# Kernel tuning notes

Hardware: AMD Instinct MI355X
Metric: run time of the kernel (lower is better)

Reference implementation:

```python
import jax, jax.numpy as jnp
import numpy as np


def grid_sample_bilinear(feat, grid):
    """Bilinear grid_sample, align_corners=False, zeros padding.
    feat: [B, C, H, W]; grid: [B, N, 2] with (x, y) in [-1, 1]. Returns [B, C, N].
    """
    B, C, H, W = feat.shape
    gx, gy = grid[..., 0], grid[..., 1]
    # unnormalize (align_corners=False): pixel = ((g + 1) * size - 1) / 2
    ix = ((gx + 1.0) * W - 1.0) * 0.5
    iy = ((gy + 1.0) * H - 1.0) * 0.5
    x0 = jnp.floor(ix)
    y0 = jnp.floor(iy)
    x1 = x0 + 1.0
    y1 = y0 + 1.0
    wx1 = ix - x0
    wx0 = 1.0 - wx1
    wy1 = iy - y0
    wy0 = 1.0 - wy1
    featf = feat.reshape(B, C, H * W)

    def corner(xi, yi, w):
        valid = (xi >= 0) & (xi <= W - 1) & (yi >= 0) & (yi <= H - 1)
        xi_c = jnp.clip(xi, 0, W - 1).astype(jnp.int32)
        yi_c = jnp.clip(yi, 0, H - 1).astype(jnp.int32)
        idx = yi_c * W + xi_c                                  # [B, N]
        vals = jnp.take_along_axis(featf, idx[:, None, :], axis=2)  # [B, C, N]
        return vals * (w * valid.astype(feat.dtype))[:, None, :]

    return (corner(x0, y0, wx0 * wy0) + corner(x1, y0, wx1 * wy0)
            + corner(x0, y1, wx0 * wy1) + corner(x1, y1, wx1 * wy1))


def setup_inputs() -> dict:
    key = jax.random.key(0)
    ks = jax.random.split(key, 8)
    B_T, C, H, W = 128, 256, 64, 64
    J = 17
    n_heads, n_points = 8, 4
    HP = n_heads * n_points
    video_features = jax.random.normal(ks[0], (B_T, C, H, W), dtype=jnp.float32)
    reference_points = jax.random.uniform(ks[1], (B_T, J, 2), dtype=jnp.float32,
                                          minval=-1.0, maxval=1.0)
    # offset predictor: Linear(C -> HP*2); weights init small like the module
    W_off = 0.01 * jax.random.normal(ks[2], (C, HP * 2), dtype=jnp.float32)
    b_off = 0.01 * jax.random.normal(ks[3], (HP * 2,), dtype=jnp.float32)
    # weight predictor: Linear(C -> HP)
    W_w = 0.01 * jax.random.normal(ks[4], (C, HP), dtype=jnp.float32)
    b_w = jnp.zeros((HP,), dtype=jnp.float32)
    # output projection: Linear(C -> C), xavier-ish scale
    W_out = jax.random.normal(ks[5], (C, C), dtype=jnp.float32) * (1.0 / np.sqrt(C))
    b_out = jnp.zeros((C,), dtype=jnp.float32)
    return {"video_features": video_features, "reference_points": reference_points,
            "W_off": W_off, "b_off": b_off, "W_w": W_w, "b_w": b_w,
            "W_out": W_out, "b_out": b_out}


def reference(video_features, reference_points, W_off, b_off, W_w, b_w, W_out, b_out):
    B, C, H, W = video_features.shape
    J = reference_points.shape[1]
    HP = W_w.shape[1]  # n_heads * n_points
    # initial queries: sample features at reference points -> [B, J, C]
    q = grid_sample_bilinear(video_features, reference_points).transpose(0, 2, 1)
    # learned fractional offsets: [B, J, HP, 2]
    offsets = (q @ W_off + b_off).reshape(B, J, HP, 2)
    # softmax attention weights over all heads*points: [B, J, HP]
    weights = jax.nn.softmax(q @ W_w + b_w, axis=-1)
    # final sampling grid, clamped to valid range: [B, J*HP, 2]
    grid = jnp.clip(reference_points[:, :, None, :] + offsets, -1.0, 1.0)
    grid = grid.reshape(B, J * HP, 2)
    # sample and weighted-sum: [B, C, J, HP] x [B, J, HP] -> [B, J, C]
    sampled = grid_sample_bilinear(video_features, grid).reshape(B, C, J, HP)
    out = jnp.einsum('bcjp,bjp->bjc', sampled, weights)
    return out @ W_out + b_out
```

## Files before the change

### kernel.cpp

```cpp
#include <hip/hip_runtime.h>

#define B_  128
#define C_  256
#define H_  64
#define W_  64
#define J_  17
#define HP_ 32
#define HW_ (H_ * W_)
#define CG_ 4

__global__ __launch_bounds__(256)
void pass12_kernel(const float* __restrict__ feat,
                   const float* __restrict__ refpts,
                   const float* __restrict__ Woff,
                   const float* __restrict__ boff,
                   const float* __restrict__ Ww,
                   const float* __restrict__ bw,
                   int4*  __restrict__ meta_idx,
                   float4* __restrict__ meta_w)
{
    __shared__ float q_lds[C_];
    __shared__ float part_off[4][64];
    __shared__ float part_w[8][32];
    __shared__ float off_lds[2 * HP_];
    __shared__ float logit_lds[HP_];

    const int bj = blockIdx.x;
    const int b  = bj / J_;
    const int j  = bj % J_;
    const int c  = threadIdx.x;

    const float rx = refpts[(b * J_ + j) * 2 + 0];
    const float ry = refpts[(b * J_ + j) * 2 + 1];

    {
        const float* featbc = feat + (size_t)(b * C_ + c) * HW_;
        float ix = (rx + 1.0f) * (0.5f * W_) - 0.5f;
        float iy = (ry + 1.0f) * (0.5f * H_) - 0.5f;
        float x0f = floorf(ix), y0f = floorf(iy);
        int x0 = (int)x0f, y0 = (int)y0f;
        int x1 = x0 + 1,  y1 = y0 + 1;
        float wx1 = ix - x0f, wx0 = 1.0f - wx1;
        float wy1 = iy - y0f, wy0 = 1.0f - wy1;
        bool vx0 = (x0 >= 0) && (x0 < W_);
        bool vx1 = (x1 >= 0) && (x1 < W_);
        bool vy0 = (y0 >= 0) && (y0 < H_);
        bool vy1 = (y1 >= 0) && (y1 < H_);
        int x0c = min(max(x0, 0), W_ - 1), x1c = min(max(x1, 0), W_ - 1);
        int y0c = min(max(y0, 0), H_ - 1), y1c = min(max(y1, 0), H_ - 1);
        float v00 = (vx0 && vy0) ? featbc[y0c * W_ + x0c] : 0.0f;
        float v10 = (vx1 && vy0) ? featbc[y0c * W_ + x1c] : 0.0f;
        float v01 = (vx0 && vy1) ? featbc[y1c * W_ + x0c] : 0.0f;
        float v11 = (vx1 && vy1) ? featbc[y1c * W_ + x1c] : 0.0f;
        q_lds[c] = v00 * (wx0 * wy0) + v10 * (wx1 * wy0)
                 + v01 * (wx0 * wy1) + v11 * (wx1 * wy1);
    }
    __syncthreads();

    {
        const int wv = c >> 6, ln = c & 63;
        float aoff = 0.0f;
        #pragma unroll 8
        for (int i = 0; i < 64; ++i) {
            const int k = wv * 64 + i;
            aoff += q_lds[k] * Woff[k * 64 + ln];
        }
        part_off[wv][ln] = aoff;
        const int h = ln >> 5, p = ln & 31;
        float aw = 0.0f;
        #pragma unroll 8
        for (int i = 0; i < 32; ++i) {
            const int k = wv * 64 + h * 32 + i;
            aw += q_lds[k] * Ww[k * 32 + p];
        }
        part_w[wv * 2 + h][p] = aw;
    }
    __syncthreads();
    if (c < 64) {
        off_lds[c] = boff[c] + part_off[0][c] + part_off[1][c]
                   + part_off[2][c] + part_off[3][c];
    } else if (c < 96) {
        const int p = c - 64;
        float s = bw[p];
        #pragma unroll
        for (int sidx = 0; sidx < 8; ++sidx) s += part_w[sidx][p];
        logit_lds[p] = s;
    }
    __syncthreads();

    if (c < HP_) {
        float l = logit_lds[c];
        float m = l;
        #pragma unroll
        for (int mask = 16; mask >= 1; mask >>= 1) m = fmaxf(m, __shfl_xor(m, mask));
        float e = expf(l - m);
        float s = e;
        #pragma unroll
        for (int mask = 16; mask >= 1; mask >>= 1) s += __shfl_xor(s, mask);
        const float ww = e / s;

        float gx = fminf(fmaxf(rx + off_lds[2 * c + 0], -1.0f), 1.0f);
        float gy = fminf(fmaxf(ry + off_lds[2 * c + 1], -1.0f), 1.0f);
        float ix = (gx + 1.0f) * (0.5f * W_) - 0.5f;
        float iy = (gy + 1.0f) * (0.5f * H_) - 0.5f;
        float x0f = floorf(ix), y0f = floorf(iy);
        int x0 = (int)x0f, y0 = (int)y0f;
        int x1 = x0 + 1,  y1 = y0 + 1;
        float wx1 = ix - x0f, wx0 = 1.0f - wx1;
        float wy1 = iy - y0f, wy0 = 1.0f - wy1;
        float v00 = (float)((x0 >= 0) && (x0 < W_) && (y0 >= 0) && (y0 < H_));
        float v10 = (float)((x1 >= 0) && (x1 < W_) && (y0 >= 0) && (y0 < H_));
        float v01 = (float)((x0 >= 0) && (x0 < W_) && (y1 >= 0) && (y1 < H_));
        float v11 = (float)((x1 >= 0) && (x1 < W_) && (y1 >= 0) && (y1 < H_));
        int x0c = min(max(x0, 0), W_ - 1), x1c = min(max(x1, 0), W_ - 1);
        int y0c = min(max(y0, 0), H_ - 1), y1c = min(max(y1, 0), H_ - 1);
        const int mi = bj * HP_ + c;
        meta_idx[mi] = make_int4(y0c * W_ + x0c, y0c * W_ + x1c,
                                 y1c * W_ + x0c, y1c * W_ + x1c);
        meta_w[mi] = make_float4(ww * wx0 * wy0 * v00, ww * wx1 * wy0 * v10,
                                 ww * wx0 * wy1 * v01, ww * wx1 * wy1 * v11);
    }
}

__global__ __launch_bounds__(512)
void gather_kernel(const float* __restrict__ feat,
                   const int4*  __restrict__ meta_idx,
                   const float4* __restrict__ meta_w,
                   float* __restrict__ acc)
{
    __shared__ float plane[CG_ * HW_];

    const int blk = blockIdx.x;
    const int b   = blk >> 6;
    const int cg  = blk & 63;
    const int c0  = cg * CG_;
    const int t   = threadIdx.x;
    const int wv  = t >> 6;
    const int ln  = t & 63;

    {
        const char* gsrc = (const char*)(feat + (size_t)(b * C_ + c0) * HW_);
        #pragma unroll
        for (int i = 0; i < 8; ++i) {
            const size_t off = ((size_t)(i * 512 + wv * 64)) * 16;
            __builtin_amdgcn_global_load_lds(
                (const __attribute__((address_space(1))) void*)(gsrc + off + (size_t)ln * 16),
                (__attribute__((address_space(3))) void*)((char*)plane + off),
                16, 0, 0);
        }
    }

    const int p    = ln & 31;
    const int half = ln >> 5;
    int4   id_r[2];
    float4 w_r[2];
    #pragma unroll
    for (int iter = 0; iter < 2; ++iter) {
        const int j = iter * 16 + wv * 2 + half;
        if (j < J_) {
            const int mi = (b * J_ + j) * HP_ + p;
            id_r[iter] = meta_idx[mi];
            w_r[iter]  = meta_w[mi];
        } else {
            id_r[iter] = make_int4(0, 0, 0, 0);
            w_r[iter]  = make_float4(0.f, 0.f, 0.f, 0.f);
        }
    }
    __syncthreads();

    #pragma unroll
    for (int iter = 0; iter < 2; ++iter) {
        const int j = iter * 16 + wv * 2 + half;
        const int4   id = id_r[iter];
        const float4 w  = w_r[iter];
        float pj0 = w.x * plane[0 * HW_ + id.x] + w.y * plane[0 * HW_ + id.y]
                  + w.z * plane[0 * HW_ + id.z] + w.w * plane[0 * HW_ + id.w];
        float pj1 = w.x * plane[1 * HW_ + id.x] + w.y * plane[1 * HW_ + id.y]
                  + w.z * plane[1 * HW_ + id.z] + w.w * plane[1 * HW_ + id.w];
        float pj2 = w.x * plane[2 * HW_ + id.x] + w.y * plane[2 * HW_ + id.y]
                  + w.z * plane[2 * HW_ + id.z] + w.w * plane[2 * HW_ + id.w];
        float pj3 = w.x * plane[3 * HW_ + id.x] + w.y * plane[3 * HW_ + id.y]
                  + w.z * plane[3 * HW_ + id.z] + w.w * plane[3 * HW_ + id.w];
        #pragma unroll
        for (int mask = 16; mask >= 1; mask >>= 1) {
            pj0 += __shfl_xor(pj0, mask);
            pj1 += __shfl_xor(pj1, mask);
            pj2 += __shfl_xor(pj2, mask);
            pj3 += __shfl_xor(pj3, mask);
        }
        if (j < J_ && p == 0) {
            float4* dst = (float4*)(acc + ((size_t)(b * J_ + j)) * C_ + c0);
            *dst = make_float4(pj0, pj1, pj2, pj3);
        }
    }
}

#define PROJ_ROWS 8
__global__ __launch_bounds__(256)
void proj_kernel(const float* __restrict__ acc,
                 const float* __restrict__ Wout,
                 const float* __restrict__ bout,
                 float* __restrict__ out)
{
    __shared__ float a_lds[PROJ_ROWS][C_];
    const int bj0 = blockIdx.x * PROJ_ROWS;
    const int t   = threadIdx.x;

    #pragma unroll
    for (int r = 0; r < PROJ_ROWS; ++r)
        a_lds[r][t] = acc[(size_t)(bj0 + r) * C_ + t];
    __syncthreads();

    const int c = t;
    float o[PROJ_ROWS];
    const float bb = bout[c];
    #pragma unroll
    for (int r = 0; r < PROJ_ROWS; ++r) o[r] = bb;

    #pragma unroll 4
    for (int k = 0; k < C_; ++k) {
        const float wv = Wout[(size_t)k * C_ + c];
        #pragma unroll
        for (int r = 0; r < PROJ_ROWS; ++r)
            o[r] += a_lds[r][k] * wv;
    }

    #pragma unroll
    for (int r = 0; r < PROJ_ROWS; ++r)
        out[(size_t)(bj0 + r) * C_ + c] = o[r];
}

__device__ __forceinline__ float bilin_sample(const float* __restrict__ featc,
                                              float gx, float gy) {
    float ix = (gx + 1.0f) * (0.5f * W_) - 0.5f;
    float iy = (gy + 1.0f) * (0.5f * H_) - 0.5f;
    float x0f = floorf(ix), y0f = floorf(iy);
    int x0 = (int)x0f, y0 = (int)y0f;
    int x1 = x0 + 1,  y1 = y0 + 1;
    float wx1 = ix - x0f, wx0 = 1.0f - wx1;
    float wy1 = iy - y0f, wy0 = 1.0f - wy1;
    bool vx0 = (x0 >= 0) && (x0 < W_);
    bool vx1 = (x1 >= 0) && (x1 < W_);
    bool vy0 = (y0 >= 0) && (y0 < H_);
    bool vy1 = (y1 >= 0) && (y1 < H_);
    int x0c = min(max(x0, 0), W_ - 1), x1c = min(max(x1, 0), W_ - 1);
    int y0c = min(max(y0, 0), H_ - 1), y1c = min(max(y1, 0), H_ - 1);
    float v00 = (vx0 && vy0) ? featc[y0c * W_ + x0c] : 0.0f;
    float v10 = (vx1 && vy0) ? featc[y0c * W_ + x1c] : 0.0f;
    float v01 = (vx0 && vy1) ? featc[y1c * W_ + x0c] : 0.0f;
    float v11 = (vx1 && vy1) ? featc[y1c * W_ + x1c] : 0.0f;
    return v00 * (wx0 * wy0) + v10 * (wx1 * wy0)
         + v01 * (wx0 * wy1) + v11 * (wx1 * wy1);
}

__global__ __launch_bounds__(256)
void msdks_kernel(const float* __restrict__ feat,
                  const float* __restrict__ refpts,
                  const float* __restrict__ Woff,
                  const float* __restrict__ boff,
                  const float* __restrict__ Ww,
                  const float* __restrict__ bw,
                  const float* __restrict__ Wout,
                  const float* __restrict__ bout,
                  float* __restrict__ out)
{
    __shared__ float q_lds[C_];
    __shared__ float off_lds[2 * HP_];
    __shared__ float logit_lds[HP_];
    __shared__ float wgt_lds[HP_];
    __shared__ float gx_lds[HP_];
    __shared__ float gy_lds[HP_];
    __shared__ float acc_lds[C_];

    const int bj = blockIdx.x;
    const int b  = bj / J_;
    const int j  = bj % J_;
    const int c  = threadIdx.x;

    const float rx = refpts[(b * J_ + j) * 2 + 0];
    const float ry = refpts[(b * J_ + j) * 2 + 1];
    const float* featbc = feat + (size_t)(b * C_ + c) * HW_;

    q_lds[c] = bilin_sample(featbc, rx, ry);
    __syncthreads();

    if (c < 64) {
        float s = boff[c];
        for (int k = 0; k < C_; ++k) s += q_lds[k] * Woff[k * 64 + c];
        off_lds[c] = s;
    } else if (c < 96) {
        const int p = c - 64;
        float s = bw[p];
        for (int k = 0; k < C_; ++k) s += q_lds[k] * Ww[k * HP_ + p];
        logit_lds[p] = s;
    }
    __syncthreads();

    if (c < HP_) {
        float l = logit_lds[c];
        float m = l;
        for (int mask = 16; mask; mask >>= 1) m = fmaxf(m, __shfl_xor(m, mask));
        float e = expf(l - m);
        float s = e;
        for (int mask = 16; mask; mask >>= 1) s += __shfl_xor(s, mask);
        wgt_lds[c] = e / s;
        gx_lds[c] = fminf(fmaxf(rx + off_lds[c * 2 + 0], -1.0f), 1.0f);
        gy_lds[c] = fminf(fmaxf(ry + off_lds[c * 2 + 1], -1.0f), 1.0f);
    }
    __syncthreads();

    float acc = 0.0f;
    for (int pp = 0; pp < HP_; ++pp)
        acc += wgt_lds[pp] * bilin_sample(featbc, gx_lds[pp], gy_lds[pp]);
    acc_lds[c] = acc;
    __syncthreads();

    float o = bout[c];
    for (int k = 0; k < C_; ++k) o += acc_lds[k] * Wout[k * C_ + c];
    out[(size_t)(b * J_ + j) * C_ + c] = o;
}

extern "C" void kernel_launch(void* const* d_in, const int* in_sizes, int n_in,
                              void* d_out, int out_size, void* d_ws, size_t ws_size,
                              hipStream_t stream) {
    const float* feat   = (const float*)d_in[0];
    const float* refpts = (const float*)d_in[1];
    const float* Woff   = (const float*)d_in[2];
    const float* boff   = (const float*)d_in[3];
    const float* Ww     = (const float*)d_in[4];
    const float* bw     = (const float*)d_in[5];
    const float* Wout   = (const float*)d_in[6];
    const float* bout   = (const float*)d_in[7];
    float* out = (float*)d_out;

    const size_t n_meta    = (size_t)B_ * J_ * HP_;
    const size_t idx_bytes = n_meta * sizeof(int4);
    const size_t w_bytes   = n_meta * sizeof(float4);
    const size_t acc_bytes = (size_t)B_ * J_ * C_ * sizeof(float);

    if (ws_size >= idx_bytes + w_bytes + acc_bytes) {
        char* ws = (char*)d_ws;
        int4*   meta_idx = (int4*)ws;
        float4* meta_w   = (float4*)(ws + idx_bytes);
        float*  acc      = (float*)(ws + idx_bytes + w_bytes);

        pass12_kernel<<<dim3(B_ * J_), dim3(256), 0, stream>>>(
            feat, refpts, Woff, boff, Ww, bw, meta_idx, meta_w);
        gather_kernel<<<dim3(B_ * (C_ / CG_)), dim3(512), 0, stream>>>(
            feat, meta_idx, meta_w, acc);
        proj_kernel<<<dim3((B_ * J_) / PROJ_ROWS), dim3(256), 0, stream>>>(
            acc, Wout, bout, out);
    } else {
        msdks_kernel<<<dim3(B_ * J_), dim3(256), 0, stream>>>(
            feat, refpts, Woff, boff, Ww, bw, Wout, bout, out);
    }
}
```

Measured before the change: 155.6 us.

## Fuse three passes into a persistent cooperative kernel with double-buffered plane staging

Replaces the three separate launches (meta computation, gather, projection) with one cooperative persistent kernel of 512 blocks that uses grid-wide syncs between phases. The first feature-plane stage is issued before the meta phase so its load overlaps that computation. During the gather phase, async global-to-LDS loads of the next two-channel task are double-buffered against the current one. The aim is to remove launch gaps and hide feature-load latency, at the cost of grid-sync overhead, a smaller channel group per task, and occupancy limits from about 64KB of LDS per block.

```diff
diff --git a/kernel.cpp b/kernel.cpp
--- a/kernel.cpp
+++ b/kernel.cpp
@@ -1,4 +1,7 @@
 #include <hip/hip_runtime.h>
+#include <hip/hip_cooperative_groups.h>
+
+namespace cg = cooperative_groups;
 
 #define B_  128
 #define C_  256
@@ -7,7 +10,244 @@
 #define J_  17
 #define HP_ 32
 #define HW_ (H_ * W_)
-#define CG_ 4
+#define CG_ 2
+#define GRID_ 512
+#define TPB_  256
+#define NTASK (B_ * (C_ / CG_))
+#define TASKS_PER_BLK (NTASK / GRID_)
+#define PROJ_ROWS 8
+
+__device__ __forceinline__ void stage_task(const float* __restrict__ feat,
+                                           int task, float* buf, int t) {
+    const int b   = task >> 7;
+    const int cgp = task & 127;
+    const int wv  = t >> 6;
+    const char* gsrc = (const char*)(feat + (size_t)(b * C_ + cgp * CG_) * HW_);
+    #pragma unroll
+    for (int i = 0; i < 8; ++i) {
+        const size_t off = ((size_t)(i * 256 + wv * 64)) * 16;
+        __builtin_amdgcn_global_load_lds(
+            (const __attribute__((address_space(1))) void*)(gsrc + off + (size_t)(t & 63) * 16),
+            (__attribute__((address_space(3))) void*)((char*)buf + off),
+            16, 0, 0);
+    }
+}
+
+__global__ __launch_bounds__(TPB_, 2)
+void fused_kernel(const float* __restrict__ feat,
+                  const float* __restrict__ refpts,
+                  const float* __restrict__ Woff,
+                  const float* __restrict__ boff,
+                  const float* __restrict__ Ww,
+                  const float* __restrict__ bw,
+                  const float* __restrict__ Wout,
+                  const float* __restrict__ bout,
+                  int4*   __restrict__ meta_idx,
+                  float4* __restrict__ meta_w,
+                  float*  __restrict__ acc,
+                  float*  __restrict__ out)
+{
+    __shared__ float lds[2 * CG_ * HW_];
+    cg::grid_group grid = cg::this_grid();
+
+    const int blk = blockIdx.x;
+    const int t   = threadIdx.x;
+    const int wv  = t >> 6;
+    const int ln  = t & 63;
+
+    stage_task(feat, blk, lds, t);
+
+    {
+        float* scratch  = lds + CG_ * HW_;
+        float* q_lds    = scratch;
+        float* part_off = scratch + 256;
+        float* part_w   = scratch + 512;
+        float* off_lds  = scratch + 768;
+        float* logit    = scratch + 832;
+
+        const int nbj = (blk < (B_ * J_ - 4 * GRID_)) ? 5 : 4;
+        for (int r = 0; r < nbj; ++r) {
+            const int bj = blk + r * GRID_;
+            const int b  = bj / J_;
+            const int j  = bj % J_;
+            const int c  = t;
+
+            const float rx = refpts[(b * J_ + j) * 2 + 0];
+            const float ry = refpts[(b * J_ + j) * 2 + 1];
+
+            {
+                const float* featbc = feat + (size_t)(b * C_ + c) * HW_;
+                float ix = (rx + 1.0f) * (0.5f * W_) - 0.5f;
+                float iy = (ry + 1.0f) * (0.5f * H_) - 0.5f;
+                float x0f = floorf(ix), y0f = floorf(iy);
+                int x0 = (int)x0f, y0 = (int)y0f;
+                int x1 = x0 + 1,  y1 = y0 + 1;
+                float wx1 = ix - x0f, wx0 = 1.0f - wx1;
+                float wy1 = iy - y0f, wy0 = 1.0f - wy1;
+                bool vx0 = (x0 >= 0) && (x0 < W_);
+                bool vx1 = (x1 >= 0) && (x1 < W_);
+                bool vy0 = (y0 >= 0) && (y0 < H_);
+                bool vy1 = (y1 >= 0) && (y1 < H_);
+                int x0c = min(max(x0, 0), W_ - 1), x1c = min(max(x1, 0), W_ - 1);
+                int y0c = min(max(y0, 0), H_ - 1), y1c = min(max(y1, 0), H_ - 1);
+                float v00 = (vx0 && vy0) ? featbc[y0c * W_ + x0c] : 0.0f;
+                float v10 = (vx1 && vy0) ? featbc[y0c * W_ + x1c] : 0.0f;
+                float v01 = (vx0 && vy1) ? featbc[y1c * W_ + x0c] : 0.0f;
+                float v11 = (vx1 && vy1) ? featbc[y1c * W_ + x1c] : 0.0f;
+                q_lds[c] = v00 * (wx0 * wy0) + v10 * (wx1 * wy0)
+                         + v01 * (wx0 * wy1) + v11 * (wx1 * wy1);
+            }
+            __syncthreads();
+
+            {
+                float aoff = 0.0f;
+                #pragma unroll 8
+                for (int i = 0; i < 64; ++i) {
+                    const int k = wv * 64 + i;
+                    aoff += q_lds[k] * Woff[k * 64 + ln];
+                }
+                part_off[wv * 64 + ln] = aoff;
+                const int h = ln >> 5, p = ln & 31;
+                float aw = 0.0f;
+                #pragma unroll 8
+                for (int i = 0; i < 32; ++i) {
+                    const int k = wv * 64 + h * 32 + i;
+                    aw += q_lds[k] * Ww[k * 32 + p];
+                }
+                part_w[(wv * 2 + h) * 32 + p] = aw;
+            }
+            __syncthreads();
+            if (t < 64) {
+                off_lds[t] = boff[t] + part_off[t] + part_off[64 + t]
+                           + part_off[128 + t] + part_off[192 + t];
+            } else if (t < 96) {
+                const int p = t - 64;
+                float s = bw[p];
+                #pragma unroll
+                for (int sidx = 0; sidx < 8; ++sidx) s += part_w[sidx * 32 + p];
+                logit[p] = s;
+            }
+            __syncthreads();
+
+            if (t < HP_) {
+                float l = logit[t];
+                float m = l;
+                #pragma unroll
+                for (int mask = 16; mask >= 1; mask >>= 1) m = fmaxf(m, __shfl_xor(m, mask));
+                float e = expf(l - m);
+                float s = e;
+                #pragma unroll
+                for (int mask = 16; mask >= 1; mask >>= 1) s += __shfl_xor(s, mask);
+                const float ww = e / s;
+
+                float gx = fminf(fmaxf(rx + off_lds[2 * t + 0], -1.0f), 1.0f);
+                float gy = fminf(fmaxf(ry + off_lds[2 * t + 1], -1.0f), 1.0f);
+                float ix = (gx + 1.0f) * (0.5f * W_) - 0.5f;
+                float iy = (gy + 1.0f) * (0.5f * H_) - 0.5f;
+                float x0f = floorf(ix), y0f = floorf(iy);
+                int x0 = (int)x0f, y0 = (int)y0f;
+                int x1 = x0 + 1,  y1 = y0 + 1;
+                float wx1 = ix - x0f, wx0 = 1.0f - wx1;
+                float wy1 = iy - y0f, wy0 = 1.0f - wy1;
+                float v00 = (float)((x0 >= 0) && (x0 < W_) && (y0 >= 0) && (y0 < H_));
+                float v10 = (float)((x1 >= 0) && (x1 < W_) && (y0 >= 0) && (y0 < H_));
+                float v01 = (float)((x0 >= 0) && (x0 < W_) && (y1 >= 0) && (y1 < H_));
+                float v11 = (float)((x1 >= 0) && (x1 < W_) && (y1 >= 0) && (y1 < H_));
+                int x0c = min(max(x0, 0), W_ - 1), x1c = min(max(x1, 0), W_ - 1);
+                int y0c = min(max(y0, 0), H_ - 1), y1c = min(max(y1, 0), H_ - 1);
+                const int mi = bj * HP_ + t;
+                meta_idx[mi] = make_int4(y0c * W_ + x0c, y0c * W_ + x1c,
+                                         y1c * W_ + x0c, y1c * W_ + x1c);
+                meta_w[mi] = make_float4(ww * wx0 * wy0 * v00, ww * wx1 * wy0 * v10,
+                                         ww * wx0 * wy1 * v01, ww * wx1 * wy1 * v11);
+            }
+            __syncthreads();
+        }
+    }
+
+    __threadfence();
+    grid.sync();
+
+    const int p    = ln & 31;
+    const int half = ln >> 5;
+    for (int r = 0; r < TASKS_PER_BLK; ++r) {
+        const int task = blk + r * GRID_;
+        const int b    = task >> 7;
+        const int c0   = (task & 127) * CG_;
+        float* cur = lds + (r & 1) * (CG_ * HW_);
+
+        int4   id_r[3];
+        float4 w_r[3];
+        #pragma unroll
+        for (int iter = 0; iter < 3; ++iter) {
+            const int j = iter * 8 + wv * 2 + half;
+            if (j < J_) {
+                const int mi = (b * J_ + j) * HP_ + p;
+                id_r[iter] = meta_idx[mi];
+                w_r[iter]  = meta_w[mi];
+            } else {
+                id_r[iter] = make_int4(0, 0, 0, 0);
+                w_r[iter]  = make_float4(0.f, 0.f, 0.f, 0.f);
+            }
+        }
+
+        if (r + 1 < TASKS_PER_BLK) {
+            stage_task(feat, task + GRID_, lds + ((r + 1) & 1) * (CG_ * HW_), t);
+            asm volatile("s_waitcnt vmcnt(14)" ::: "memory");
+        } else {
+            asm volatile("s_waitcnt vmcnt(0)" ::: "memory");
+        }
+        __syncthreads();
+
+        #pragma unroll
+        for (int iter = 0; iter < 3; ++iter) {
+            const int j = iter * 8 + wv * 2 + half;
+            const int4   id = id_r[iter];
+            const float4 w  = w_r[iter];
+            float pj0 = w.x * cur[id.x] + w.y * cur[id.y]
+                      + w.z * cur[id.z] + w.w * cur[id.w];
+            float pj1 = w.x * cur[HW_ + id.x] + w.y * cur[HW_ + id.y]
+                      + w.z * cur[HW_ + id.z] + w.w * cur[HW_ + id.w];
+            #pragma unroll
+            for (int mask = 16; mask >= 1; mask >>= 1) {
+                pj0 += __shfl_xor(pj0, mask);
+                pj1 += __shfl_xor(pj1, mask);
+            }
+            if (j < J_ && p == 0) {
+                float2* dst = (float2*)(acc + ((size_t)(b * J_ + j)) * C_ + c0);
+                *dst = make_float2(pj0, pj1);
+            }
+        }
+        __syncthreads();
+    }
+
+    __threadfence();
+    grid.sync();
+
+    if (blk < (B_ * J_) / PROJ_ROWS) {
+        float* a_lds = lds;
+        const int bj0 = blk * PROJ_ROWS;
+        #pragma unroll
+        for (int r = 0; r < PROJ_ROWS; ++r)
+            a_lds[r * C_ + t] = acc[(size_t)(bj0 + r) * C_ + t];
+        __syncthreads();
+
+        float o[PROJ_ROWS];
+        const float bb = bout[t];
+        #pragma unroll
+        for (int r = 0; r < PROJ_ROWS; ++r) o[r] = bb;
+        #pragma unroll 4
+        for (int k = 0; k < C_; ++k) {
+            const float wvv = Wout[(size_t)k * C_ + t];
+            #pragma unroll
+            for (int r = 0; r < PROJ_ROWS; ++r)
+                o[r] += a_lds[r * C_ + k] * wvv;
+        }
+        #pragma unroll
+        for (int r = 0; r < PROJ_ROWS; ++r)
+            out[(size_t)(bj0 + r) * C_ + t] = o[r];
+    }
+}
 
 __global__ __launch_bounds__(256)
 void pass12_kernel(const float* __restrict__ feat,
@@ -128,12 +368,12 @@
                    const float4* __restrict__ meta_w,
                    float* __restrict__ acc)
 {
-    __shared__ float plane[CG_ * HW_];
+    __shared__ float plane[4 * HW_];
 
     const int blk = blockIdx.x;
     const int b   = blk >> 6;
     const int cg  = blk & 63;
-    const int c0  = cg * CG_;
+    const int c0  = cg * 4;
     const int t   = threadIdx.x;
     const int wv  = t >> 6;
     const int ln  = t & 63;
@@ -195,7 +435,6 @@
     }
 }
 
-#define PROJ_ROWS 8
 __global__ __launch_bounds__(256)
 void proj_kernel(const float* __restrict__ acc,
                  const float* __restrict__ Wout,
@@ -211,113 +450,20 @@
         a_lds[r][t] = acc[(size_t)(bj0 + r) * C_ + t];
     __syncthreads();
 
-    const int c = t;
     float o[PROJ_ROWS];
-    const float bb = bout[c];
+    const float bb = bout[t];
     #pragma unroll
     for (int r = 0; r < PROJ_ROWS; ++r) o[r] = bb;
-
     #pragma unroll 4
     for (int k = 0; k < C_; ++k) {
-        const float wv = Wout[(size_t)k * C_ + c];
+        const float wvv = Wout[(size_t)k * C_ + t];
         #pragma unroll
         for (int r = 0; r < PROJ_ROWS; ++r)
-            o[r] += a_lds[r][k] * wv;
-    }
-
+            o[r] += a_lds[r][k] * wvv;
+    }
     #pragma unroll
     for (int r = 0; r < PROJ_ROWS; ++r)
-        out[(size_t)(bj0 + r) * C_ + c] = o[r];
-}
-
-__device__ __forceinline__ float bilin_sample(const float* __restrict__ featc,
-                                              float gx, float gy) {
-    float ix = (gx + 1.0f) * (0.5f * W_) - 0.5f;
-    float iy = (gy + 1.0f) * (0.5f * H_) - 0.5f;
-    float x0f = floorf(ix), y0f = floorf(iy);
-    int x0 = (int)x0f, y0 = (int)y0f;
-    int x1 = x0 + 1,  y1 = y0 + 1;
-    float wx1 = ix - x0f, wx0 = 1.0f - wx1;
-    float wy1 = iy - y0f, wy0 = 1.0f - wy1;
-    bool vx0 = (x0 >= 0) && (x0 < W_);
-    bool vx1 = (x1 >= 0) && (x1 < W_);
-    bool vy0 = (y0 >= 0) && (y0 < H_);
-    bool vy1 = (y1 >= 0) && (y1 < H_);
-    int x0c = min(max(x0, 0), W_ - 1), x1c = min(max(x1, 0), W_ - 1);
-    int y0c = min(max(y0, 0), H_ - 1), y1c = min(max(y1, 0), H_ - 1);
-    float v00 = (vx0 && vy0) ? featc[y0c * W_ + x0c] : 0.0f;
-    float v10 = (vx1 && vy0) ? featc[y0c * W_ + x1c] : 0.0f;
-    float v01 = (vx0 && vy1) ? featc[y1c * W_ + x0c] : 0.0f;
-    float v11 = (vx1 && vy1) ? featc[y1c * W_ + x1c] : 0.0f;
-    return v00 * (wx0 * wy0) + v10 * (wx1 * wy0)
-         + v01 * (wx0 * wy1) + v11 * (wx1 * wy1);
-}
-
-__global__ __launch_bounds__(256)
-void msdks_kernel(const float* __restrict__ feat,
-                  const float* __restrict__ refpts,
-                  const float* __restrict__ Woff,
-                  const float* __restrict__ boff,
-                  const float* __restrict__ Ww,
-                  const float* __restrict__ bw,
-                  const float* __restrict__ Wout,
-                  const float* __restrict__ bout,
-                  float* __restrict__ out)
-{
-    __shared__ float q_lds[C_];
-    __shared__ float off_lds[2 * HP_];
-    __shared__ float logit_lds[HP_];
-    __shared__ float wgt_lds[HP_];
-    __shared__ float gx_lds[HP_];
-    __shared__ float gy_lds[HP_];
-    __shared__ float acc_lds[C_];
-
-    const int bj = blockIdx.x;
-    const int b  = bj / J_;
-    const int j  = bj % J_;
-    const int c  = threadIdx.x;
-
-    const float rx = refpts[(b * J_ + j) * 2 + 0];
-    const float ry = refpts[(b * J_ + j) * 2 + 1];
-    const float* featbc = feat + (size_t)(b * C_ + c) * HW_;
-
-    q_lds[c] = bilin_sample(featbc, rx, ry);
-    __syncthreads();
-
-    if (c < 64) {
-        float s = boff[c];
-        for (int k = 0; k < C_; ++k) s += q_lds[k] * Woff[k * 64 + c];
-        off_lds[c] = s;
-    } else if (c < 96) {
-        const int p = c - 64;
-        float s = bw[p];
-        for (int k = 0; k < C_; ++k) s += q_lds[k] * Ww[k * HP_ + p];
-        logit_lds[p] = s;
-    }
-    __syncthreads();
-
-    if (c < HP_) {
-        float l = logit_lds[c];
-        float m = l;
-        for (int mask = 16; mask; mask >>= 1) m = fmaxf(m, __shfl_xor(m, mask));
-        float e = expf(l - m);
-        float s = e;
-        for (int mask = 16; mask; mask >>= 1) s += __shfl_xor(s, mask);
-        wgt_lds[c] = e / s;
-        gx_lds[c] = fminf(fmaxf(rx + off_lds[c * 2 + 0], -1.0f), 1.0f);
-        gy_lds[c] = fminf(fmaxf(ry + off_lds[c * 2 + 1], -1.0f), 1.0f);
-    }
-    __syncthreads();
-
-    float acc = 0.0f;
-    for (int pp = 0; pp < HP_; ++pp)
-        acc += wgt_lds[pp] * bilin_sample(featbc, gx_lds[pp], gy_lds[pp]);
-    acc_lds[c] = acc;
-    __syncthreads();
-
-    float o = bout[c];
-    for (int k = 0; k < C_; ++k) o += acc_lds[k] * Wout[k * C_ + c];
-    out[(size_t)(b * J_ + j) * C_ + c] = o;
+        out[(size_t)(bj0 + r) * C_ + t] = o[r];
 }
 
 extern "C" void kernel_launch(void* const* d_in, const int* in_sizes, int n_in,
@@ -337,21 +483,31 @@
     const size_t idx_bytes = n_meta * sizeof(int4);
     const size_t w_bytes   = n_meta * sizeof(float4);
     const size_t acc_bytes = (size_t)B_ * J_ * C_ * sizeof(float);
-
-    if (ws_size >= idx_bytes + w_bytes + acc_bytes) {
-        char* ws = (char*)d_ws;
-        int4*   meta_idx = (int4*)ws;
-        float4* meta_w   = (float4*)(ws + idx_bytes);
-        float*  acc      = (float*)(ws + idx_bytes + w_bytes);
-
-        pass12_kernel<<<dim3(B_ * J_), dim3(256), 0, stream>>>(
-            feat, refpts, Woff, boff, Ww, bw, meta_idx, meta_w);
-        gather_kernel<<<dim3(B_ * (C_ / CG_)), dim3(512), 0, stream>>>(
-            feat, meta_idx, meta_w, acc);
-        proj_kernel<<<dim3((B_ * J_) / PROJ_ROWS), dim3(256), 0, stream>>>(
-            acc, Wout, bout, out);
-    } else {
-        msdks_kernel<<<dim3(B_ * J_), dim3(256), 0, stream>>>(
-            feat, refpts, Woff, boff, Ww, bw, Wout, bout, out);
-    }
+    if (ws_size < idx_bytes + w_bytes + acc_bytes) return;
+
+    char* ws = (char*)d_ws;
+    int4*   meta_idx = (int4*)ws;
+    float4* meta_w   = (float4*)(ws + idx_bytes);
+    float*  acc      = (float*)(ws + idx_bytes + w_bytes);
+
+    int nb = 0;
+    bool coop = (hipOccupancyMaxActiveBlocksPerMultiprocessor(
+                     &nb, (const void*)fused_kernel, TPB_, 0) == hipSuccess) && nb >= 2;
+
+    if (coop) {
+        void* args[] = {(void*)&feat, (void*)&refpts, (void*)&Woff, (void*)&boff,
+                        (void*)&Ww,   (void*)&bw,     (void*)&Wout, (void*)&bout,
+                        (void*)&meta_idx, (void*)&meta_w, (void*)&acc, (void*)&out};
+        hipError_t e = hipLaunchCooperativeKernel((const void*)fused_kernel,
+                                                  dim3(GRID_), dim3(TPB_),
+                                                  args, 0, stream);
+        if (e == hipSuccess) return;
+    }
+
+    pass12_kernel<<<dim3(B_ * J_), dim3(256), 0, stream>>>(
+        feat, refpts, Woff, boff, Ww, bw, meta_idx, meta_w);
+    gather_kernel<<<dim3(B_ * 64), dim3(512), 0, stream>>>(
+        feat, meta_idx, meta_w, acc);
+    proj_kernel<<<dim3((B_ * J_) / PROJ_ROWS), dim3(256), 0, stream>>>(
+        acc, Wout, bout, out);
 }
```

New measurement: 402.9 us. 159% more time.
